# Performance work log

Hardware: AMD Instinct MI355X
Metric: run time of the kernel (lower is better)

Reference implementation:

```python
import jax, jax.numpy as jnp
import numpy as np

B, N = 1, 768
C_A, C_S, C_Z = 768, 384, 128
H, C_HID, N_TRANS = 16, 48, 2
INF = 1e9
PNAMES = ['attn_s_ln_g', 'attn_ada_gate_w', 'attn_ada_gate_b', 'attn_ada_skip_w',
          'wq', 'bq', 'wk', 'wv', 'z_ln_g', 'z_ln_b', 'wb', 'wg', 'wo',
          'attn_out_gate_w', 'attn_out_gate_b',
          'tr_s_ln_g', 'tr_ada_gate_w', 'tr_ada_gate_b', 'tr_ada_skip_w',
          'tr_w1', 'tr_w2', 'tr_wo', 'tr_out_gate_w', 'tr_out_gate_b']


def _ln(x, eps=1e-5):
    mu = jnp.mean(x, axis=-1, keepdims=True)
    var = jnp.mean((x - mu) ** 2, axis=-1, keepdims=True)
    return (x - mu) * jax.lax.rsqrt(var + eps)


def _adaln(a, s, s_g, gate_w, gate_b, skip_w):
    # AF3 Algorithm 26 AdaLN: a <- LN(a, no affine); s <- LN(s, scale only)
    a_ln = _ln(a)
    s_ln = _ln(s) * s_g
    return jax.nn.sigmoid(s_ln @ gate_w + gate_b) * a_ln + s_ln @ skip_w


def setup_inputs() -> dict:
    key = jax.random.key(0)
    ks = iter(jax.random.split(key, 40))
    w = lambda *sh: jax.random.normal(next(ks), sh, jnp.float32) * 0.02
    return dict(
        a=jax.random.normal(next(ks), (B, N, C_A), jnp.float32),
        s=jax.random.normal(next(ks), (B, N, C_S), jnp.float32),
        z=jax.random.normal(next(ks), (B, N, N, C_Z), jnp.float32),
        mask=jnp.ones((B, N), jnp.int32),
        attn_s_ln_g=jnp.ones((C_S,), jnp.float32),
        attn_ada_gate_w=w(C_S, C_A),
        attn_ada_gate_b=jnp.zeros((C_A,), jnp.float32),
        attn_ada_skip_w=w(C_S, C_A),
        wq=w(C_A, H * C_HID), bq=jnp.zeros((H * C_HID,), jnp.float32),
        wk=w(C_A, H * C_HID), wv=w(C_A, H * C_HID),
        z_ln_g=jnp.ones((C_Z,), jnp.float32), z_ln_b=jnp.zeros((C_Z,), jnp.float32),
        wb=w(C_Z, H), wg=w(C_A, H * C_HID), wo=w(H * C_HID, C_A),
        attn_out_gate_w=w(C_S, C_A),
        attn_out_gate_b=jnp.full((C_A,), -2.0, jnp.float32),  # AdaLN-Zero bias init -2
        tr_s_ln_g=jnp.ones((C_S,), jnp.float32),
        tr_ada_gate_w=w(C_S, C_A),
        tr_ada_gate_b=jnp.zeros((C_A,), jnp.float32),
        tr_ada_skip_w=w(C_S, C_A),
        tr_w1=w(C_A, N_TRANS * C_A), tr_w2=w(C_A, N_TRANS * C_A),
        tr_wo=w(N_TRANS * C_A, C_A),
        tr_out_gate_w=w(C_S, C_A),
        tr_out_gate_b=jnp.full((C_A,), -2.0, jnp.float32),
    )


def _block(a, s, z, maskf, p):
    # --- AttentionPairBias (AF3 Alg 24), residual ---
    a_ln = _adaln(a, s, p['attn_s_ln_g'], p['attn_ada_gate_w'],
                  p['attn_ada_gate_b'], p['attn_ada_skip_w'])
    q = (a_ln @ p['wq'] + p['bq']).reshape(B, N, H, C_HID)
    k = (a_ln @ p['wk']).reshape(B, N, H, C_HID)
    v = (a_ln @ p['wv']).reshape(B, N, H, C_HID)
    pair_bias = (_ln(z) * p['z_ln_g'] + p['z_ln_b']) @ p['wb']  # [B,N,N,H]
    logits = jnp.einsum('bqhc,bkhc->bhqk', q, k) / np.float32(np.sqrt(C_HID))
    logits = logits + jnp.moveaxis(pair_bias, -1, 1)
    logits = logits + (maskf - 1.0)[:, None, None, :] * INF  # mask over keys
    attn = jax.nn.softmax(logits, axis=-1)
    o = jnp.einsum('bhqk,bkhc->bqhc', attn, v)
    g = jax.nn.sigmoid(a_ln @ p['wg']).reshape(B, N, H, C_HID)
    o = (o * g).reshape(B, N, H * C_HID) @ p['wo']
    o = jax.nn.sigmoid(s @ p['attn_out_gate_w'] + p['attn_out_gate_b']) * o
    a = a + o
    # --- ConditionedTransitionBlock (AF3 Alg 25, SwiGLU), residual ---
    t_ln = _adaln(a, s, p['tr_s_ln_g'], p['tr_ada_gate_w'],
                  p['tr_ada_gate_b'], p['tr_ada_skip_w'])
    hid = jax.nn.silu(t_ln @ p['tr_w1']) * (t_ln @ p['tr_w2'])
    t = jax.nn.sigmoid(s @ p['tr_out_gate_w'] + p['tr_out_gate_b']) * (hid @ p['tr_wo'])
    t = t * maskf[..., None]  # _mask_trans=True
    return a + t


def reference(a, s, z, mask, attn_s_ln_g, attn_ada_gate_w, attn_ada_gate_b,
              attn_ada_skip_w, wq, bq, wk, wv, z_ln_g, z_ln_b, wb, wg, wo,
              attn_out_gate_w, attn_out_gate_b, tr_s_ln_g, tr_ada_gate_w,
              tr_ada_gate_b, tr_ada_skip_w, tr_w1, tr_w2, tr_wo,
              tr_out_gate_w, tr_out_gate_b):
    p = dict(zip(PNAMES, (attn_s_ln_g, attn_ada_gate_w, attn_ada_gate_b,
                          attn_ada_skip_w, wq, bq, wk, wv, z_ln_g, z_ln_b, wb,
                          wg, wo, attn_out_gate_w, attn_out_gate_b, tr_s_ln_g,
                          tr_ada_gate_w, tr_ada_gate_b, tr_ada_skip_w, tr_w1,
                          tr_w2, tr_wo, tr_out_gate_w, tr_out_gate_b)))
    return _block(a, s, z, mask.astype(a.dtype), p)
```

## Files before the change

### kernel.cpp

```cpp
#include <hip/hip_runtime.h>
#include <hip/hip_bf16.h>
#include <stdint.h>


typedef __bf16 bf16x8 __attribute__((ext_vector_type(8)));
typedef float  f32x4  __attribute__((ext_vector_type(4)));

#define DEVI __device__ __forceinline__

DEVI uint16_t f2b(float f){ __hip_bfloat16 h = __float2bfloat16(f); return __builtin_bit_cast(uint16_t, h); }
DEVI float    b2f(uint16_t u){ return __bfloat162float(__builtin_bit_cast(__hip_bfloat16, u)); }
DEVI float    sigm(float x){ return 1.0f/(1.0f + __expf(-x)); }

DEVI f32x4 MFMA(uint4 a, uint4 b, f32x4 c){
  return __builtin_amdgcn_mfma_f32_16x16x32_bf16(
      __builtin_bit_cast(bf16x8, a), __builtin_bit_cast(bf16x8, b), c, 0, 0, 0);
}

constexpr size_t SZ_BT_ADA   = (size_t)1536*384*2;
constexpr size_t OFF_BT_ADA_ATTN = 0;
constexpr size_t OFF_BT_ADA_TR   = OFF_BT_ADA_ATTN + SZ_BT_ADA;
constexpr size_t OFF_BT_OUTGATE  = OFF_BT_ADA_TR   + SZ_BT_ADA;
constexpr size_t OFF_BT_QKVG     = OFF_BT_OUTGATE  + SZ_BT_ADA;
constexpr size_t OFF_BT_WO       = OFF_BT_QKVG + (size_t)3072*768*2;
constexpr size_t OFF_BT_W12      = OFF_BT_WO   + (size_t)768*768*2;
constexpr size_t OFF_BT_TRWO     = OFF_BT_W12  + (size_t)3072*768*2;
constexpr size_t OFF_WBGT        = OFF_BT_TRWO + (size_t)768*1536*2;
constexpr size_t OFF_ZCOL        = OFF_WBGT + 4096;
constexpr size_t OFF_OGB         = OFF_ZCOL + 256;
constexpr size_t OFF_SBF         = OFF_OGB + 6144;
constexpr size_t OFF_SLNA        = OFF_SBF  + (size_t)768*384*2;
constexpr size_t OFF_SLNT        = OFF_SLNA + (size_t)768*384*2;
constexpr size_t OFF_ALNRAW      = OFF_SLNT + (size_t)768*384*2;
constexpr size_t OFF_GATEOUT     = OFF_ALNRAW + (size_t)768*768*4;
constexpr size_t OFF_GS          = OFF_GATEOUT + (size_t)768*1536*4;
constexpr size_t OFF_ALNBF       = OFF_GS + (size_t)768*1536*4;
constexpr size_t OFF_QKVG        = OFF_ALNBF + (size_t)768*768*2;
constexpr size_t OFF_QP          = OFF_QKVG + (size_t)768*3072*4;
constexpr size_t OFF_KP          = OFF_QP + (size_t)16*768*64*2;
constexpr size_t OFF_VT          = OFF_KP + (size_t)16*768*64*2;
constexpr size_t OFF_BIAS        = OFF_VT + (size_t)16*64*768*2;
constexpr size_t OFF_SP          = OFF_BIAS + (size_t)16*768*768*2;
constexpr size_t OFF_OBF         = OFF_SP + (size_t)16*768*768*2;
constexpr size_t OFF_AMID        = OFF_OBF + (size_t)768*768*2;

struct CvtArgs {
  const float* src[14];
  uint16_t*    dst[14];
  int K[14], N[14];
  int prefix[15];
};

__global__ __launch_bounds__(256) void k_cvt(CvtArgs a){
  int bid = blockIdx.x;
  int ti = 0;
  while (ti < 13 && bid >= a.prefix[ti+1]) ti++;
  int local = bid - a.prefix[ti];
  int K = a.K[ti], N = a.N[ti];
  int tN = N >> 5;
  int n0 = (local % tN) << 5, k0 = (local / tN) << 5;
  __shared__ float lds[32][33];
  const float* src = a.src[ti];
  uint16_t* dst = a.dst[ti];
  int t = threadIdx.x;
  int c = t & 31, r0 = t >> 5;
  #pragma unroll
  for (int i = 0; i < 4; i++){
    int kk = r0 + 8*i;
    lds[kk][c] = src[(size_t)(k0+kk)*N + n0 + c];
  }
  __syncthreads();
  #pragma unroll
  for (int i = 0; i < 4; i++){
    int nn = r0 + 8*i;
    dst[(size_t)(n0+nn)*K + k0 + c] = f2b(lds[c][nn]);
  }
}

__global__ __launch_bounds__(128) void k_prep(
    const float* s, const float* g_attn, const float* g_tr,
    const float* attn_ogb, const float* tr_ogb,
    const float* z_g, const float* z_b, const float* wb,
    uint16_t* s_bf, uint16_t* sln_a, uint16_t* sln_t,
    float* ogb, uint16_t* wbgt, float* zcol)
{
  int b = blockIdx.x, t = threadIdx.x;
  if (b < 768){
    const float* row = s + (size_t)b*384;
    float x0 = row[t], x1 = row[t+128], x2 = row[t+256];
    float sm = x0+x1+x2, sq = x0*x0+x1*x1+x2*x2;
    #pragma unroll
    for (int off = 32; off; off >>= 1){ sm += __shfl_xor(sm, off, 64); sq += __shfl_xor(sq, off, 64); }
    __shared__ float rs_[2], rq_[2];
    int w = t >> 6;
    if ((t & 63) == 0){ rs_[w] = sm; rq_[w] = sq; }
    __syncthreads();
    float S = rs_[0]+rs_[1], Q = rq_[0]+rq_[1];
    float mu = S * (1.f/384.f);
    float var = Q * (1.f/384.f) - mu*mu;
    float rstd = rsqrtf(var + 1e-5f);
    float xs[3] = {x0, x1, x2};
    #pragma unroll
    for (int i = 0; i < 3; i++){
      int ci = t + 128*i;
      float ln = (xs[i] - mu) * rstd;
      s_bf [(size_t)b*384 + ci] = f2b(xs[i]);
      sln_a[(size_t)b*384 + ci] = f2b(ln * g_attn[ci]);
      sln_t[(size_t)b*384 + ci] = f2b(ln * g_tr[ci]);
    }
  } else if (b == 768){
    for (int i = t; i < 1536; i += 128)
      ogb[i] = (i < 768) ? attn_ogb[i] : tr_ogb[i-768];
  } else {
    for (int i = t; i < 2048; i += 128){
      int h = i >> 7, c = i & 127;
      wbgt[i] = f2b(z_g[c] * wb[c*16 + h]);
    }
    if (t < 16){
      float cs = 0.f, cn = 0.f;
      for (int c = 0; c < 128; c++){ cs += z_g[c]*wb[c*16+t]; cn += z_b[c]*wb[c*16+t]; }
      zcol[t] = cs; zcol[16+t] = cn;
    }
  }
}

__global__ __launch_bounds__(256) void k_ln768(const float* in, float* out){
  int b = blockIdx.x, t = threadIdx.x;
  const float* row = in + (size_t)b*768;
  float x0 = row[t], x1 = row[t+256], x2 = row[t+512];
  float sm = x0+x1+x2, sq = x0*x0+x1*x1+x2*x2;
  #pragma unroll
  for (int off = 32; off; off >>= 1){ sm += __shfl_xor(sm, off, 64); sq += __shfl_xor(sq, off, 64); }
  __shared__ float rs_[4], rq_[4];
  int w = t >> 6;
  if ((t & 63) == 0){ rs_[w] = sm; rq_[w] = sq; }
  __syncthreads();
  float S = rs_[0]+rs_[1]+rs_[2]+rs_[3], Q = rq_[0]+rq_[1]+rq_[2]+rq_[3];
  float mu = S*(1.f/768.f), var = Q*(1.f/768.f) - mu*mu, rstd = rsqrtf(var + 1e-5f);
  float* orow = out + (size_t)b*768;
  orow[t]     = (x0-mu)*rstd;
  orow[t+256] = (x1-mu)*rstd;
  orow[t+512] = (x2-mu)*rstd;
}

__global__ __launch_bounds__(256) void k_gemm(
    const uint16_t* __restrict__ A, const uint16_t* __restrict__ BT,
    int M, int N, int K,
    float* outF, uint16_t* outB, int mode,
    const float* bias, const float* gate, int gateLd, int gateOff,
    const float* resid, const int* mask)
{
  constexpr int SA = 40;
  __shared__ uint16_t As[64*SA], Bs[64*SA];
  int t = threadIdx.x;
  int n0 = blockIdx.x*64, m0 = blockIdx.y*64;
  int w = t >> 6, lane = t & 63, mm = lane & 15, q = lane >> 4;
  f32x4 zz = {0.f, 0.f, 0.f, 0.f};
  f32x4 acc[4] = {zz, zz, zz, zz};
  int r = t >> 2, c4 = t & 3;
  const uint4* Ag = (const uint4*)(A + (size_t)(m0 + r)*K) + c4;
  const uint4* Bg = (const uint4*)(BT + (size_t)(n0 + r)*K) + c4;
  for (int k0 = 0; k0 < K; k0 += 32){
    *(uint4*)&As[r*SA + c4*8] = Ag[k0 >> 3];
    *(uint4*)&Bs[r*SA + c4*8] = Bg[k0 >> 3];
    __syncthreads();
    uint4 av = *(const uint4*)&As[(16*w + mm)*SA + q*8];
    #pragma unroll
    for (int j = 0; j < 4; j++){
      uint4 bv = *(const uint4*)&Bs[(16*j + mm)*SA + q*8];
      acc[j] = MFMA(av, bv, acc[j]);
    }
    __syncthreads();
  }
  #pragma unroll
  for (int j = 0; j < 4; j++){
    #pragma unroll
    for (int rr = 0; rr < 4; rr++){
      int row = m0 + 16*w + q*4 + rr;
      int col = n0 + 16*j + mm;
      float v = acc[j][rr];
      size_t oi = (size_t)row*N + col;
      if (mode == 0)      outF[oi] = v;
      else if (mode == 1) outB[oi] = f2b(v);
      else if (mode == 2) outF[oi] = sigm(v + bias[col]);
      else if (mode == 5) outF[oi] = resid[oi] + gate[(size_t)row*gateLd + gateOff + col]*v;
      else {
        float mf = (float)mask[row];
        outF[oi] = resid[oi] + mf * gate[(size_t)row*gateLd + gateOff + col] * v;
      }
    }
  }
}

__global__ __launch_bounds__(256) void k_zbias(
    const float* __restrict__ z, const uint16_t* __restrict__ wbgt_g,
    const float* __restrict__ zcol, uint16_t* __restrict__ bias_g)
{
  __shared__ uint16_t zb[64*128];
  __shared__ uint16_t wbt[16*128];
  __shared__ float mu_s[64], rs_s[64];
  __shared__ uint16_t Sout[16*72];
  int t = threadIdx.x;
  size_t P0 = (size_t)blockIdx.y*768 + (size_t)blockIdx.x*64;
  ((uint4*)wbt)[t] = ((const uint4*)wbgt_g)[t];
  int p = t >> 2, qq = t & 3;
  const float4* zp = (const float4*)(z + (P0 + p)*128) + qq*8;
  float s1 = 0.f, s2 = 0.f;
  uint32_t lb[16];
  #pragma unroll
  for (int it = 0; it < 8; it++){
    float4 v = zp[it];
    s1 += v.x + v.y + v.z + v.w;
    s2 += v.x*v.x + v.y*v.y + v.z*v.z + v.w*v.w;
    lb[2*it]   = (uint32_t)f2b(v.x) | ((uint32_t)f2b(v.y) << 16);
    lb[2*it+1] = (uint32_t)f2b(v.z) | ((uint32_t)f2b(v.w) << 16);
  }
  uint4* zb4 = (uint4*)zb;
  #pragma unroll
  for (int kk = 0; kk < 4; kk++)
    zb4[p*16 + qq*4 + kk] = ((uint4*)lb)[kk];
  s1 += __shfl_xor(s1, 1, 64); s1 += __shfl_xor(s1, 2, 64);
  s2 += __shfl_xor(s2, 1, 64); s2 += __shfl_xor(s2, 2, 64);
  if (qq == 0){
    float mu = s1 * (1.f/128.f);
    mu_s[p] = mu;
    rs_s[p] = rsqrtf(s2*(1.f/128.f) - mu*mu + 1e-5f);
  }
  __syncthreads();
  int w = t >> 6, lane = t & 63, hh = lane & 15, q = lane >> 4;
  float cs = zcol[hh], cn = zcol[16 + hh];
  f32x4 acc = {0.f, 0.f, 0.f, 0.f};
  const uint4* wbt4 = (const uint4*)wbt;
  #pragma unroll
  for (int kc = 0; kc < 4; kc++){
    uint4 av = zb4[(16*w + hh)*16 + kc*4 + q];
    uint4 bv = wbt4[hh*16 + kc*4 + q];
    acc = MFMA(av, bv, acc);
  }
  #pragma unroll
  for (int rr = 0; rr < 4; rr++){
    int pl = 16*w + q*4 + rr;
    float val = rs_s[pl]*(acc[rr] - mu_s[pl]*cs) + cn;
    Sout[hh*72 + pl] = f2b(val);
  }
  __syncthreads();
  int h2 = t >> 4, p2 = (t & 15)*4;
  uint2 v2 = *(uint2*)&Sout[h2*72 + p2];
  *(uint2*)(bias_g + (size_t)h2*589824 + P0 + p2) = v2;
}

__global__ __launch_bounds__(256) void k_trans(
    const float* __restrict__ qkvg, const float* __restrict__ bq,
    uint16_t* qp, uint16_t* kp, uint16_t* vt)
{
  int h = blockIdx.y, n0 = blockIdx.x*64, t = threadIdx.x;
  __shared__ uint16_t vbuf[64*72];
  int c = t & 63, r0 = t >> 6;
  const float scale = 0.14433756729740643f;
  for (int r = r0; r < 64; r += 4){
    size_t base = (size_t)(n0 + r)*3072;
    float qv = 0.f, kv = 0.f, vv = 0.f;
    if (c < 48){
      int cc = h*48 + c;
      qv = (qkvg[base + cc] + bq[cc]) * scale;
      kv = qkvg[base + 768 + cc];
      vv = qkvg[base + 1536 + cc];
    }
    size_t oi = ((size_t)h*768 + n0 + r)*64 + c;
    qp[oi] = f2b(qv);
    kp[oi] = f2b(kv);
    vbuf[c*72 + r] = f2b(vv);
  }
  __syncthreads();
  int cc = t >> 2, rb = (t & 3)*16;
  uint16_t* dst = vt + ((size_t)h*64 + cc)*768 + n0 + rb;
  *(uint4*)dst       = *(uint4*)&vbuf[cc*72 + rb];
  *(uint4*)(dst + 8) = *(uint4*)&vbuf[cc*72 + rb + 8];
}

__global__ __launch_bounds__(256) void k_logits(
    const uint16_t* __restrict__ qp, const uint16_t* __restrict__ kp,
    const uint16_t* __restrict__ bias_g, const int* __restrict__ mask,
    uint16_t* __restrict__ SP)
{
  int h = blockIdx.z, q0 = blockIdx.y*64, k0 = blockIdx.x*64;
  constexpr int SA = 72;
  __shared__ uint16_t Qs[64*SA], Ks[64*SA];
  int t = threadIdx.x;
  int r = t >> 2, c4 = t & 3;
  const uint4* Qg = (const uint4*)(qp + ((size_t)h*768 + q0 + r)*64);
  const uint4* Kg = (const uint4*)(kp + ((size_t)h*768 + k0 + r)*64);
  *(uint4*)&Qs[r*SA + c4*8]       = Qg[c4];
  *(uint4*)&Qs[r*SA + (c4+4)*8]   = Qg[c4+4];
  *(uint4*)&Ks[r*SA + c4*8]       = Kg[c4];
  *(uint4*)&Ks[r*SA + (c4+4)*8]   = Kg[c4+4];
  __syncthreads();
  int w = t >> 6, lane = t & 63, mm = lane & 15, q = lane >> 4;
  f32x4 zz = {0.f,0.f,0.f,0.f};
  f32x4 acc[4] = {zz, zz, zz, zz};
  #pragma unroll
  for (int kc = 0; kc < 2; kc++){
    uint4 av = *(const uint4*)&Qs[(16*w + mm)*SA + kc*32 + q*8];
    #pragma unroll
    for (int j = 0; j < 4; j++){
      uint4 bv = *(const uint4*)&Ks[(16*j + mm)*SA + kc*32 + q*8];
      acc[j] = MFMA(av, bv, acc[j]);
    }
  }
  #pragma unroll
  for (int j = 0; j < 4; j++){
    #pragma unroll
    for (int rr = 0; rr < 4; rr++){
      int row = q0 + 16*w + q*4 + rr;
      int col = k0 + 16*j + mm;
      size_t bi = (size_t)h*589824 + (size_t)row*768 + col;
      float v = acc[j][rr] + b2f(bias_g[bi]) + ((float)mask[col] - 1.f)*1e9f;
      SP[bi] = f2b(v);
    }
  }
}

__global__ __launch_bounds__(256) void k_softmax(uint16_t* SP){
  size_t base = (size_t)blockIdx.x * 768;
  int t = threadIdx.x;
  float x0 = b2f(SP[base+t]), x1 = b2f(SP[base+t+256]), x2 = b2f(SP[base+t+512]);
  float mx = fmaxf(x0, fmaxf(x1, x2));
  #pragma unroll
  for (int off = 32; off; off >>= 1) mx = fmaxf(mx, __shfl_xor(mx, off, 64));
  __shared__ float rm[4], rsum[4];
  int w = t >> 6;
  if ((t & 63) == 0) rm[w] = mx;
  __syncthreads();
  mx = fmaxf(fmaxf(rm[0], rm[1]), fmaxf(rm[2], rm[3]));
  float e0 = __expf(x0 - mx), e1 = __expf(x1 - mx), e2 = __expf(x2 - mx);
  float sm = e0 + e1 + e2;
  #pragma unroll
  for (int off = 32; off; off >>= 1) sm += __shfl_xor(sm, off, 64);
  if ((t & 63) == 0) rsum[w] = sm;
  __syncthreads();
  sm = rsum[0]+rsum[1]+rsum[2]+rsum[3];
  float inv = 1.f / sm;
  SP[base+t]     = f2b(e0*inv);
  SP[base+t+256] = f2b(e1*inv);
  SP[base+t+512] = f2b(e2*inv);
}

__global__ __launch_bounds__(256) void k_pv(
    const uint16_t* __restrict__ SP, const uint16_t* __restrict__ vt,
    const float* __restrict__ qkvg, uint16_t* __restrict__ obf)
{
  int h = blockIdx.y, q0 = blockIdx.x*64;
  constexpr int SA = 40;
  __shared__ uint16_t Ps[64*SA], Vs[64*SA];
  int t = threadIdx.x;
  int r = t >> 2, c4 = t & 3;
  int w = t >> 6, lane = t & 63, mm = lane & 15, q = lane >> 4;
  const uint16_t* Pbase = SP + (size_t)h*589824;
  const uint16_t* Vbase = vt + (size_t)h*64*768;
  f32x4 zz = {0.f,0.f,0.f,0.f};
  f32x4 acc[3] = {zz, zz, zz};
  for (int k0 = 0; k0 < 768; k0 += 32){
    *(uint4*)&Ps[r*SA + c4*8] = *((const uint4*)(Pbase + (size_t)(q0 + r)*768 + k0) + c4);
    *(uint4*)&Vs[r*SA + c4*8] = *((const uint4*)(Vbase + (size_t)r*768 + k0) + c4);
    __syncthreads();
    uint4 av = *(const uint4*)&Ps[(16*w + mm)*SA + q*8];
    #pragma unroll
    for (int j = 0; j < 3; j++){
      uint4 bv = *(const uint4*)&Vs[(16*j + mm)*SA + q*8];
      acc[j] = MFMA(av, bv, acc[j]);
    }
    __syncthreads();
  }
  #pragma unroll
  for (int j = 0; j < 3; j++){
    #pragma unroll
    for (int rr = 0; rr < 4; rr++){
      int col = 16*j + mm;
      if (col < 48){
        int row = q0 + 16*w + q*4 + rr;
        float g = qkvg[(size_t)row*3072 + 2304 + h*48 + col];
        obf[(size_t)row*768 + h*48 + col] = f2b(acc[j][rr] * sigm(g));
      }
    }
  }
}

__global__ __launch_bounds__(256) void k_adaln(
    const float* __restrict__ gs, const float* __restrict__ gb,
    const float* __restrict__ alnraw, uint16_t* __restrict__ aln)
{
  int idx4 = blockIdx.x*256 + threadIdx.x;
  int row = idx4 / 192;
  int c4 = (idx4 % 192)*4;
  float4 g4 = *(const float4*)(gs + (size_t)row*1536 + c4);
  float4 s4 = *(const float4*)(gs + (size_t)row*1536 + 768 + c4);
  float4 a4 = *(const float4*)(alnraw + (size_t)row*768 + c4);
  float4 b4 = *(const float4*)(gb + c4);
  uint32_t lo = (uint32_t)f2b(sigm(g4.x + b4.x)*a4.x + s4.x)
              | ((uint32_t)f2b(sigm(g4.y + b4.y)*a4.y + s4.y) << 16);
  uint32_t hi = (uint32_t)f2b(sigm(g4.z + b4.z)*a4.z + s4.z)
              | ((uint32_t)f2b(sigm(g4.w + b4.w)*a4.w + s4.w) << 16);
  uint2 uv; uv.x = lo; uv.y = hi;
  *(uint2*)(aln + (size_t)row*768 + c4) = uv;
}

__global__ __launch_bounds__(256) void k_silu(const float* __restrict__ h12, uint16_t* __restrict__ hid){
  int idx4 = blockIdx.x*256 + threadIdx.x;
  int row = idx4 / 384;
  int c4 = (idx4 % 384)*4;
  float4 x1 = *(const float4*)(h12 + (size_t)row*3072 + c4);
  float4 x2 = *(const float4*)(h12 + (size_t)row*3072 + 1536 + c4);
  uint32_t lo = (uint32_t)f2b(x1.x*sigm(x1.x)*x2.x)
              | ((uint32_t)f2b(x1.y*sigm(x1.y)*x2.y) << 16);
  uint32_t hi = (uint32_t)f2b(x1.z*sigm(x1.z)*x2.z)
              | ((uint32_t)f2b(x1.w*sigm(x1.w)*x2.w) << 16);
  uint2 uv; uv.x = lo; uv.y = hi;
  *(uint2*)(hid + (size_t)row*1536 + c4) = uv;
}

extern "C" void kernel_launch(void* const* d_in, const int* in_sizes, int n_in,
                              void* d_out, int out_size, void* d_ws, size_t ws_size,
                              hipStream_t stream)
{
  const float* a            = (const float*)d_in[0];
  const float* s            = (const float*)d_in[1];
  const float* z            = (const float*)d_in[2];
  const int*   mask         = (const int*)  d_in[3];
  const float* attn_s_ln_g  = (const float*)d_in[4];
  const float* attn_gate_w  = (const float*)d_in[5];
  const float* attn_gate_b  = (const float*)d_in[6];
  const float* attn_skip_w  = (const float*)d_in[7];
  const float* wq           = (const float*)d_in[8];
  const float* bq           = (const float*)d_in[9];
  const float* wk           = (const float*)d_in[10];
  const float* wv           = (const float*)d_in[11];
  const float* z_ln_g       = (const float*)d_in[12];
  const float* z_ln_b       = (const float*)d_in[13];
  const float* wb           = (const float*)d_in[14];
  const float* wg           = (const float*)d_in[15];
  const float* wo           = (const float*)d_in[16];
  const float* attn_og_w    = (const float*)d_in[17];
  const float* attn_og_b    = (const float*)d_in[18];
  const float* tr_s_ln_g    = (const float*)d_in[19];
  const float* tr_gate_w    = (const float*)d_in[20];
  const float* tr_gate_b    = (const float*)d_in[21];
  const float* tr_skip_w    = (const float*)d_in[22];
  const float* tr_w1        = (const float*)d_in[23];
  const float* tr_w2        = (const float*)d_in[24];
  const float* tr_wo        = (const float*)d_in[25];
  const float* tr_og_w      = (const float*)d_in[26];
  const float* tr_og_b      = (const float*)d_in[27];

  char* wsb = (char*)d_ws;
  uint16_t* BTa   = (uint16_t*)(wsb + OFF_BT_ADA_ATTN);
  uint16_t* BTt   = (uint16_t*)(wsb + OFF_BT_ADA_TR);
  uint16_t* BTo   = (uint16_t*)(wsb + OFF_BT_OUTGATE);
  uint16_t* BTq   = (uint16_t*)(wsb + OFF_BT_QKVG);
  uint16_t* BTwo  = (uint16_t*)(wsb + OFF_BT_WO);
  uint16_t* BTw12 = (uint16_t*)(wsb + OFF_BT_W12);
  uint16_t* BTtw  = (uint16_t*)(wsb + OFF_BT_TRWO);
  uint16_t* WBGT  = (uint16_t*)(wsb + OFF_WBGT);
  float*    ZCOL  = (float*)   (wsb + OFF_ZCOL);
  float*    OGB   = (float*)   (wsb + OFF_OGB);
  uint16_t* SBF   = (uint16_t*)(wsb + OFF_SBF);
  uint16_t* SLNA  = (uint16_t*)(wsb + OFF_SLNA);
  uint16_t* SLNT  = (uint16_t*)(wsb + OFF_SLNT);
  float*    ALNRAW= (float*)   (wsb + OFF_ALNRAW);
  float*    GATEOUT=(float*)   (wsb + OFF_GATEOUT);
  float*    GS    = (float*)   (wsb + OFF_GS);
  uint16_t* ALNBF = (uint16_t*)(wsb + OFF_ALNBF);
  float*    QKVG  = (float*)   (wsb + OFF_QKVG);
  uint16_t* QP    = (uint16_t*)(wsb + OFF_QP);
  uint16_t* KP    = (uint16_t*)(wsb + OFF_KP);
  uint16_t* VT    = (uint16_t*)(wsb + OFF_VT);
  uint16_t* BIASB = (uint16_t*)(wsb + OFF_BIAS);
  uint16_t* SPB   = (uint16_t*)(wsb + OFF_SP);
  uint16_t* OBF   = (uint16_t*)(wsb + OFF_OBF);
  float*    AMID  = (float*)   (wsb + OFF_AMID);
  uint16_t* HIDBF = (uint16_t*)(wsb + OFF_BIAS);
  float*    OUTF  = (float*)d_out;

  CvtArgs ca;
  const float* srcs[14] = {attn_gate_w, attn_skip_w, tr_gate_w, tr_skip_w,
                           attn_og_w, tr_og_w, wq, wk, wv, wg, wo, tr_w1, tr_w2, tr_wo};
  uint16_t* dsts[14] = {BTa, BTa + (size_t)768*384, BTt, BTt + (size_t)768*384,
                        BTo, BTo + (size_t)768*384,
                        BTq, BTq + (size_t)768*768, BTq + (size_t)2*768*768, BTq + (size_t)3*768*768,
                        BTwo, BTw12, BTw12 + (size_t)1536*768, BTtw};
  int Ks[14] = {384,384,384,384,384,384, 768,768,768,768,768, 768,768, 1536};
  int Ns[14] = {768,768,768,768,768,768, 768,768,768,768,768, 1536,1536, 768};
  int tiles[14] = {288,288,288,288,288,288, 576,576,576,576,576, 1152,1152, 1152};
  int pre = 0;
  for (int i = 0; i < 14; i++){
    ca.src[i] = srcs[i]; ca.dst[i] = dsts[i]; ca.K[i] = Ks[i]; ca.N[i] = Ns[i];
    ca.prefix[i] = pre; pre += tiles[i];
  }
  ca.prefix[14] = pre;

  k_cvt<<<pre, 256, 0, stream>>>(ca);
  k_prep<<<770, 128, 0, stream>>>(s, attn_s_ln_g, tr_s_ln_g, attn_og_b, tr_og_b,
                                  z_ln_g, z_ln_b, wb, SBF, SLNA, SLNT, OGB, WBGT, ZCOL);
  k_ln768<<<768, 256, 0, stream>>>(a, ALNRAW);

  k_gemm<<<dim3(24,12), 256, 0, stream>>>(SBF, BTo, 768, 1536, 384,
      GATEOUT, nullptr, 2, OGB, nullptr, 0, 0, nullptr, nullptr);
  k_gemm<<<dim3(24,12), 256, 0, stream>>>(SLNA, BTa, 768, 1536, 384,
      GS, nullptr, 0, nullptr, nullptr, 0, 0, nullptr, nullptr);
  k_adaln<<<576, 256, 0, stream>>>(GS, attn_gate_b, ALNRAW, ALNBF);
  k_gemm<<<dim3(48,12), 256, 0, stream>>>(ALNBF, BTq, 768, 3072, 768,
      QKVG, nullptr, 0, nullptr, nullptr, 0, 0, nullptr, nullptr);

  k_zbias<<<dim3(12,768), 256, 0, stream>>>(z, WBGT, ZCOL, BIASB);
  k_trans<<<dim3(12,16), 256, 0, stream>>>(QKVG, bq, QP, KP, VT);
  k_logits<<<dim3(12,12,16), 256, 0, stream>>>(QP, KP, BIASB, mask, SPB);
  k_softmax<<<12288, 256, 0, stream>>>(SPB);
  k_pv<<<dim3(12,16), 256, 0, stream>>>(SPB, VT, QKVG, OBF);
  k_gemm<<<dim3(12,12), 256, 0, stream>>>(OBF, BTwo, 768, 768, 768,
      AMID, nullptr, 5, nullptr, GATEOUT, 1536, 0, a, nullptr);

  k_ln768<<<768, 256, 0, stream>>>(AMID, ALNRAW);
  k_gemm<<<dim3(24,12), 256, 0, stream>>>(SLNT, BTt, 768, 1536, 384,
      GS, nullptr, 0, nullptr, nullptr, 0, 0, nullptr, nullptr);
  k_adaln<<<576, 256, 0, stream>>>(GS, tr_gate_b, ALNRAW, ALNBF);
  k_gemm<<<dim3(48,12), 256, 0, stream>>>(ALNBF, BTw12, 768, 3072, 768,
      QKVG, nullptr, 0, nullptr, nullptr, 0, 0, nullptr, nullptr);
  k_silu<<<1152, 256, 0, stream>>>(QKVG, HIDBF);
  k_gemm<<<dim3(12,12), 256, 0, stream>>>(HIDBF, BTtw, 768, 768, 1536,
      OUTF, nullptr, 4, nullptr, GATEOUT, 1536, 768, AMID, mask);
}
```

Before: 682.6 us.

## Fuse attention into flash kernel, fuse LN into AdaLN, bf16 intermediates, async GEMM loads

Result: faster. 635.3 us (-6.9%).

```diff
diff --git a/kernel.cpp b/kernel.cpp
--- a/kernel.cpp
+++ b/kernel.cpp
@@ -15,6 +15,12 @@
 DEVI f32x4 MFMA(uint4 a, uint4 b, f32x4 c){
   return __builtin_amdgcn_mfma_f32_16x16x32_bf16(
       __builtin_bit_cast(bf16x8, a), __builtin_bit_cast(bf16x8, b), c, 0, 0, 0);
+}
+
+DEVI void glds16(const void* g, void* l){
+  __builtin_amdgcn_global_load_lds(
+      (const __attribute__((address_space(1))) void*)g,
+      (__attribute__((address_space(3))) void*)l, 16, 0, 0);
 }
 
 constexpr size_t SZ_BT_ADA   = (size_t)1536*384*2;
@@ -31,17 +37,15 @@
 constexpr size_t OFF_SBF         = OFF_OGB + 6144;
 constexpr size_t OFF_SLNA        = OFF_SBF  + (size_t)768*384*2;
 constexpr size_t OFF_SLNT        = OFF_SLNA + (size_t)768*384*2;
-constexpr size_t OFF_ALNRAW      = OFF_SLNT + (size_t)768*384*2;
-constexpr size_t OFF_GATEOUT     = OFF_ALNRAW + (size_t)768*768*4;
+constexpr size_t OFF_GATEOUT     = OFF_SLNT + (size_t)768*384*2;
 constexpr size_t OFF_GS          = OFF_GATEOUT + (size_t)768*1536*4;
 constexpr size_t OFF_ALNBF       = OFF_GS + (size_t)768*1536*4;
-constexpr size_t OFF_QKVG        = OFF_ALNBF + (size_t)768*768*2;
-constexpr size_t OFF_QP          = OFF_QKVG + (size_t)768*3072*4;
+constexpr size_t OFF_QKVGB       = OFF_ALNBF + (size_t)768*768*2;
+constexpr size_t OFF_QP          = OFF_QKVGB + (size_t)768*3072*2;
 constexpr size_t OFF_KP          = OFF_QP + (size_t)16*768*64*2;
 constexpr size_t OFF_VT          = OFF_KP + (size_t)16*768*64*2;
 constexpr size_t OFF_BIAS        = OFF_VT + (size_t)16*64*768*2;
-constexpr size_t OFF_SP          = OFF_BIAS + (size_t)16*768*768*2;
-constexpr size_t OFF_OBF         = OFF_SP + (size_t)16*768*768*2;
+constexpr size_t OFF_OBF         = OFF_BIAS + (size_t)16*768*768*2;
 constexpr size_t OFF_AMID        = OFF_OBF + (size_t)768*768*2;
 
 struct CvtArgs {
@@ -124,9 +128,12 @@
   }
 }
 
-__global__ __launch_bounds__(256) void k_ln768(const float* in, float* out){
+__global__ __launch_bounds__(256) void k_adaln2(
+    const float* __restrict__ asrc, const float* __restrict__ gs,
+    const float* __restrict__ gb, uint16_t* __restrict__ out)
+{
   int b = blockIdx.x, t = threadIdx.x;
-  const float* row = in + (size_t)b*768;
+  const float* row = asrc + (size_t)b*768;
   float x0 = row[t], x1 = row[t+256], x2 = row[t+512];
   float sm = x0+x1+x2, sq = x0*x0+x1*x1+x2*x2;
   #pragma unroll
@@ -137,10 +144,14 @@
   __syncthreads();
   float S = rs_[0]+rs_[1]+rs_[2]+rs_[3], Q = rq_[0]+rq_[1]+rq_[2]+rq_[3];
   float mu = S*(1.f/768.f), var = Q*(1.f/768.f) - mu*mu, rstd = rsqrtf(var + 1e-5f);
-  float* orow = out + (size_t)b*768;
-  orow[t]     = (x0-mu)*rstd;
-  orow[t+256] = (x1-mu)*rstd;
-  orow[t+512] = (x2-mu)*rstd;
+  float xs[3] = {x0, x1, x2};
+  #pragma unroll
+  for (int i = 0; i < 3; i++){
+    int c = t + 256*i;
+    float g  = gs[(size_t)b*1536 + c];
+    float sk = gs[(size_t)b*1536 + 768 + c];
+    out[(size_t)b*768 + c] = f2b(sigm(g + gb[c]) * ((xs[i]-mu)*rstd) + sk);
+  }
 }
 
 __global__ __launch_bounds__(256) void k_gemm(
@@ -150,27 +161,40 @@
     const float* bias, const float* gate, int gateLd, int gateOff,
     const float* resid, const int* mask)
 {
-  constexpr int SA = 40;
-  __shared__ uint16_t As[64*SA], Bs[64*SA];
+  __shared__ uint16_t As[64*64], Bs[64*64];
   int t = threadIdx.x;
   int n0 = blockIdx.x*64, m0 = blockIdx.y*64;
   int w = t >> 6, lane = t & 63, mm = lane & 15, q = lane >> 4;
-  f32x4 zz = {0.f, 0.f, 0.f, 0.f};
+  int fc0 = 128*w + lane, fc1 = fc0 + 64;
+  int r0 = fc0 >> 3, c0 = (fc0 & 7) ^ (r0 & 7);
+  int r1 = fc1 >> 3, c1 = (fc1 & 7) ^ (r1 & 7);
+  const uint16_t* gA0 = A  + (size_t)(m0 + r0)*K + c0*8;
+  const uint16_t* gA1 = A  + (size_t)(m0 + r1)*K + c1*8;
+  const uint16_t* gB0 = BT + (size_t)(n0 + r0)*K + c0*8;
+  const uint16_t* gB1 = BT + (size_t)(n0 + r1)*K + c1*8;
+  uint16_t* lA0 = As + (2*w + 0)*512;
+  uint16_t* lA1 = As + (2*w + 1)*512;
+  uint16_t* lB0 = Bs + (2*w + 0)*512;
+  uint16_t* lB1 = Bs + (2*w + 1)*512;
+  f32x4 zz = {0.f,0.f,0.f,0.f};
   f32x4 acc[4] = {zz, zz, zz, zz};
-  int r = t >> 2, c4 = t & 3;
-  const uint4* Ag = (const uint4*)(A + (size_t)(m0 + r)*K) + c4;
-  const uint4* Bg = (const uint4*)(BT + (size_t)(n0 + r)*K) + c4;
-  for (int k0 = 0; k0 < K; k0 += 32){
-    *(uint4*)&As[r*SA + c4*8] = Ag[k0 >> 3];
-    *(uint4*)&Bs[r*SA + c4*8] = Bg[k0 >> 3];
+  int sw = mm & 7;
+  for (int k0 = 0; k0 < K; k0 += 64){
     __syncthreads();
-    uint4 av = *(const uint4*)&As[(16*w + mm)*SA + q*8];
-    #pragma unroll
-    for (int j = 0; j < 4; j++){
-      uint4 bv = *(const uint4*)&Bs[(16*j + mm)*SA + q*8];
-      acc[j] = MFMA(av, bv, acc[j]);
-    }
+    glds16(gA0 + k0, lA0);
+    glds16(gA1 + k0, lA1);
+    glds16(gB0 + k0, lB0);
+    glds16(gB1 + k0, lB1);
     __syncthreads();
+    #pragma unroll
+    for (int kc = 0; kc < 2; kc++){
+      uint4 av = *(const uint4*)&As[(16*w + mm)*64 + ((kc*4 + q) ^ sw)*8];
+      #pragma unroll
+      for (int j = 0; j < 4; j++){
+        uint4 bv = *(const uint4*)&Bs[(16*j + mm)*64 + ((kc*4 + q) ^ sw)*8];
+        acc[j] = MFMA(av, bv, acc[j]);
+      }
+    }
   }
   #pragma unroll
   for (int j = 0; j < 4; j++){
@@ -250,7 +274,7 @@
 }
 
 __global__ __launch_bounds__(256) void k_trans(
-    const float* __restrict__ qkvg, const float* __restrict__ bq,
+    const uint16_t* __restrict__ qkvg, const float* __restrict__ bq,
     uint16_t* qp, uint16_t* kp, uint16_t* vt)
 {
   int h = blockIdx.y, n0 = blockIdx.x*64, t = threadIdx.x;
@@ -262,9 +286,9 @@
     float qv = 0.f, kv = 0.f, vv = 0.f;
     if (c < 48){
       int cc = h*48 + c;
-      qv = (qkvg[base + cc] + bq[cc]) * scale;
-      kv = qkvg[base + 768 + cc];
-      vv = qkvg[base + 1536 + cc];
+      qv = (b2f(qkvg[base + cc]) + bq[cc]) * scale;
+      kv = b2f(qkvg[base + 768 + cc]);
+      vv = b2f(qkvg[base + 1536 + cc]);
     }
     size_t oi = ((size_t)h*768 + n0 + r)*64 + c;
     qp[oi] = f2b(qv);
@@ -278,144 +302,138 @@
   *(uint4*)(dst + 8) = *(uint4*)&vbuf[cc*72 + rb + 8];
 }
 
-__global__ __launch_bounds__(256) void k_logits(
+__global__ __launch_bounds__(256) void k_flash(
     const uint16_t* __restrict__ qp, const uint16_t* __restrict__ kp,
-    const uint16_t* __restrict__ bias_g, const int* __restrict__ mask,
-    uint16_t* __restrict__ SP)
-{
-  int h = blockIdx.z, q0 = blockIdx.y*64, k0 = blockIdx.x*64;
-  constexpr int SA = 72;
-  __shared__ uint16_t Qs[64*SA], Ks[64*SA];
+    const uint16_t* __restrict__ vt, const uint16_t* __restrict__ bias_g,
+    const uint16_t* __restrict__ qkvg, const int* __restrict__ mask,
+    uint16_t* __restrict__ obf)
+{
+  __shared__ uint16_t Qs[64*72], Ks[64*72], Vs[64*72], Ps[64*72];
+  __shared__ float mk[768];
   int t = threadIdx.x;
-  int r = t >> 2, c4 = t & 3;
-  const uint4* Qg = (const uint4*)(qp + ((size_t)h*768 + q0 + r)*64);
-  const uint4* Kg = (const uint4*)(kp + ((size_t)h*768 + k0 + r)*64);
-  *(uint4*)&Qs[r*SA + c4*8]       = Qg[c4];
-  *(uint4*)&Qs[r*SA + (c4+4)*8]   = Qg[c4+4];
-  *(uint4*)&Ks[r*SA + c4*8]       = Kg[c4];
-  *(uint4*)&Ks[r*SA + (c4+4)*8]   = Kg[c4+4];
-  __syncthreads();
+  int q0 = blockIdx.x*64, h = blockIdx.y;
   int w = t >> 6, lane = t & 63, mm = lane & 15, q = lane >> 4;
+  {
+    int row = t >> 2, c = t & 3;
+    const uint4* src = (const uint4*)(qp + ((size_t)h*768 + q0 + row)*64) + c*2;
+    *(uint4*)&Qs[row*72 + c*16]     = src[0];
+    *(uint4*)&Qs[row*72 + c*16 + 8] = src[1];
+    mk[t] = (float)mask[t]; mk[t+256] = (float)mask[t+256]; mk[t+512] = (float)mask[t+512];
+  }
   f32x4 zz = {0.f,0.f,0.f,0.f};
-  f32x4 acc[4] = {zz, zz, zz, zz};
-  #pragma unroll
-  for (int kc = 0; kc < 2; kc++){
-    uint4 av = *(const uint4*)&Qs[(16*w + mm)*SA + kc*32 + q*8];
+  f32x4 o0 = zz, o1 = zz, o2 = zz;
+  f32x4 m_i = {-1e30f,-1e30f,-1e30f,-1e30f};
+  f32x4 l_i = zz;
+  const uint16_t* bias_h = bias_g + (size_t)h*589824;
+  for (int kt = 0; kt < 12; kt++){
+    __syncthreads();
+    {
+      int row = t >> 2, c = t & 3;
+      const uint4* ks = (const uint4*)(kp + ((size_t)h*768 + kt*64 + row)*64) + c*2;
+      *(uint4*)&Ks[row*72 + c*16]     = ks[0];
+      *(uint4*)&Ks[row*72 + c*16 + 8] = ks[1];
+      const uint4* vs = (const uint4*)(vt + ((size_t)h*64 + row)*768 + kt*64) + c*2;
+      *(uint4*)&Vs[row*72 + c*16]     = vs[0];
+      *(uint4*)&Vs[row*72 + c*16 + 8] = vs[1];
+    }
+    __syncthreads();
+    f32x4 s[4] = {zz, zz, zz, zz};
+    #pragma unroll
+    for (int kc = 0; kc < 2; kc++){
+      uint4 av = *(const uint4*)&Qs[(16*w + mm)*72 + kc*32 + q*8];
+      #pragma unroll
+      for (int j = 0; j < 4; j++){
+        uint4 bv = *(const uint4*)&Ks[(16*j + mm)*72 + kc*32 + q*8];
+        s[j] = MFMA(av, bv, s[j]);
+      }
+    }
+    int srow = q0 + 16*w + q*4;
     #pragma unroll
     for (int j = 0; j < 4; j++){
-      uint4 bv = *(const uint4*)&Ks[(16*j + mm)*SA + kc*32 + q*8];
-      acc[j] = MFMA(av, bv, acc[j]);
-    }
-  }
-  #pragma unroll
-  for (int j = 0; j < 4; j++){
+      int scol = kt*64 + 16*j + mm;
+      float mt = (mk[scol] - 1.f)*1e9f;
+      #pragma unroll
+      for (int rr = 0; rr < 4; rr++)
+        s[j][rr] += b2f(bias_h[(size_t)(srow+rr)*768 + scol]) + mt;
+    }
+    f32x4 tm = s[0];
+    #pragma unroll
+    for (int j = 1; j < 4; j++)
+      #pragma unroll
+      for (int rr = 0; rr < 4; rr++) tm[rr] = fmaxf(tm[rr], s[j][rr]);
+    #pragma unroll
+    for (int off = 1; off < 16; off <<= 1)
+      #pragma unroll
+      for (int rr = 0; rr < 4; rr++) tm[rr] = fmaxf(tm[rr], __shfl_xor(tm[rr], off, 64));
+    f32x4 mnew, alpha, rsum = zz;
+    #pragma unroll
+    for (int rr = 0; rr < 4; rr++){
+      mnew[rr] = fmaxf(m_i[rr], tm[rr]);
+      alpha[rr] = __expf(m_i[rr] - mnew[rr]);
+    }
+    #pragma unroll
+    for (int j = 0; j < 4; j++)
+      #pragma unroll
+      for (int rr = 0; rr < 4; rr++){
+        s[j][rr] = __expf(s[j][rr] - mnew[rr]);
+        rsum[rr] += s[j][rr];
+      }
+    #pragma unroll
+    for (int off = 1; off < 16; off <<= 1)
+      #pragma unroll
+      for (int rr = 0; rr < 4; rr++) rsum[rr] += __shfl_xor(rsum[rr], off, 64);
+    #pragma unroll
+    for (int rr = 0; rr < 4; rr++){
+      l_i[rr] = l_i[rr]*alpha[rr] + rsum[rr];
+      o0[rr] *= alpha[rr]; o1[rr] *= alpha[rr]; o2[rr] *= alpha[rr];
+      m_i[rr] = mnew[rr];
+    }
+    #pragma unroll
+    for (int j = 0; j < 4; j++)
+      #pragma unroll
+      for (int rr = 0; rr < 4; rr++)
+        Ps[(16*w + q*4 + rr)*72 + 16*j + mm] = f2b(s[j][rr]);
+    __syncthreads();
+    #pragma unroll
+    for (int kc = 0; kc < 2; kc++){
+      uint4 av = *(const uint4*)&Ps[(16*w + mm)*72 + kc*32 + q*8];
+      uint4 bv0 = *(const uint4*)&Vs[(mm)*72      + kc*32 + q*8];
+      uint4 bv1 = *(const uint4*)&Vs[(16+mm)*72   + kc*32 + q*8];
+      uint4 bv2 = *(const uint4*)&Vs[(32+mm)*72   + kc*32 + q*8];
+      o0 = MFMA(av, bv0, o0);
+      o1 = MFMA(av, bv1, o1);
+      o2 = MFMA(av, bv2, o2);
+    }
+  }
+  f32x4 inv;
+  #pragma unroll
+  for (int rr = 0; rr < 4; rr++) inv[rr] = 1.f / l_i[rr];
+  #pragma unroll
+  for (int j = 0; j < 3; j++){
+    f32x4 ov = (j == 0) ? o0 : (j == 1) ? o1 : o2;
+    int col = 16*j + mm;
     #pragma unroll
     for (int rr = 0; rr < 4; rr++){
       int row = q0 + 16*w + q*4 + rr;
-      int col = k0 + 16*j + mm;
-      size_t bi = (size_t)h*589824 + (size_t)row*768 + col;
-      float v = acc[j][rr] + b2f(bias_g[bi]) + ((float)mask[col] - 1.f)*1e9f;
-      SP[bi] = f2b(v);
-    }
-  }
-}
-
-__global__ __launch_bounds__(256) void k_softmax(uint16_t* SP){
-  size_t base = (size_t)blockIdx.x * 768;
-  int t = threadIdx.x;
-  float x0 = b2f(SP[base+t]), x1 = b2f(SP[base+t+256]), x2 = b2f(SP[base+t+512]);
-  float mx = fmaxf(x0, fmaxf(x1, x2));
-  #pragma unroll
-  for (int off = 32; off; off >>= 1) mx = fmaxf(mx, __shfl_xor(mx, off, 64));
-  __shared__ float rm[4], rsum[4];
-  int w = t >> 6;
-  if ((t & 63) == 0) rm[w] = mx;
-  __syncthreads();
-  mx = fmaxf(fmaxf(rm[0], rm[1]), fmaxf(rm[2], rm[3]));
-  float e0 = __expf(x0 - mx), e1 = __expf(x1 - mx), e2 = __expf(x2 - mx);
-  float sm = e0 + e1 + e2;
-  #pragma unroll
-  for (int off = 32; off; off >>= 1) sm += __shfl_xor(sm, off, 64);
-  if ((t & 63) == 0) rsum[w] = sm;
-  __syncthreads();
-  sm = rsum[0]+rsum[1]+rsum[2]+rsum[3];
-  float inv = 1.f / sm;
-  SP[base+t]     = f2b(e0*inv);
-  SP[base+t+256] = f2b(e1*inv);
-  SP[base+t+512] = f2b(e2*inv);
-}
-
-__global__ __launch_bounds__(256) void k_pv(
-    const uint16_t* __restrict__ SP, const uint16_t* __restrict__ vt,
-    const float* __restrict__ qkvg, uint16_t* __restrict__ obf)
-{
-  int h = blockIdx.y, q0 = blockIdx.x*64;
-  constexpr int SA = 40;
-  __shared__ uint16_t Ps[64*SA], Vs[64*SA];
-  int t = threadIdx.x;
-  int r = t >> 2, c4 = t & 3;
-  int w = t >> 6, lane = t & 63, mm = lane & 15, q = lane >> 4;
-  const uint16_t* Pbase = SP + (size_t)h*589824;
-  const uint16_t* Vbase = vt + (size_t)h*64*768;
-  f32x4 zz = {0.f,0.f,0.f,0.f};
-  f32x4 acc[3] = {zz, zz, zz};
-  for (int k0 = 0; k0 < 768; k0 += 32){
-    *(uint4*)&Ps[r*SA + c4*8] = *((const uint4*)(Pbase + (size_t)(q0 + r)*768 + k0) + c4);
-    *(uint4*)&Vs[r*SA + c4*8] = *((const uint4*)(Vbase + (size_t)r*768 + k0) + c4);
-    __syncthreads();
-    uint4 av = *(const uint4*)&Ps[(16*w + mm)*SA + q*8];
-    #pragma unroll
-    for (int j = 0; j < 3; j++){
-      uint4 bv = *(const uint4*)&Vs[(16*j + mm)*SA + q*8];
-      acc[j] = MFMA(av, bv, acc[j]);
-    }
-    __syncthreads();
-  }
-  #pragma unroll
-  for (int j = 0; j < 3; j++){
-    #pragma unroll
-    for (int rr = 0; rr < 4; rr++){
-      int col = 16*j + mm;
-      if (col < 48){
-        int row = q0 + 16*w + q*4 + rr;
-        float g = qkvg[(size_t)row*3072 + 2304 + h*48 + col];
-        obf[(size_t)row*768 + h*48 + col] = f2b(acc[j][rr] * sigm(g));
-      }
-    }
-  }
-}
-
-__global__ __launch_bounds__(256) void k_adaln(
-    const float* __restrict__ gs, const float* __restrict__ gb,
-    const float* __restrict__ alnraw, uint16_t* __restrict__ aln)
-{
-  int idx4 = blockIdx.x*256 + threadIdx.x;
-  int row = idx4 / 192;
-  int c4 = (idx4 % 192)*4;
-  float4 g4 = *(const float4*)(gs + (size_t)row*1536 + c4);
-  float4 s4 = *(const float4*)(gs + (size_t)row*1536 + 768 + c4);
-  float4 a4 = *(const float4*)(alnraw + (size_t)row*768 + c4);
-  float4 b4 = *(const float4*)(gb + c4);
-  uint32_t lo = (uint32_t)f2b(sigm(g4.x + b4.x)*a4.x + s4.x)
-              | ((uint32_t)f2b(sigm(g4.y + b4.y)*a4.y + s4.y) << 16);
-  uint32_t hi = (uint32_t)f2b(sigm(g4.z + b4.z)*a4.z + s4.z)
-              | ((uint32_t)f2b(sigm(g4.w + b4.w)*a4.w + s4.w) << 16);
-  uint2 uv; uv.x = lo; uv.y = hi;
-  *(uint2*)(aln + (size_t)row*768 + c4) = uv;
-}
-
-__global__ __launch_bounds__(256) void k_silu(const float* __restrict__ h12, uint16_t* __restrict__ hid){
+      float g = b2f(qkvg[(size_t)row*3072 + 2304 + h*48 + col]);
+      obf[(size_t)row*768 + h*48 + col] = f2b(ov[rr]*inv[rr]*sigm(g));
+    }
+  }
+}
+
+__global__ __launch_bounds__(256) void k_silu(const uint16_t* __restrict__ h12, uint16_t* __restrict__ hid){
   int idx4 = blockIdx.x*256 + threadIdx.x;
   int row = idx4 / 384;
   int c4 = (idx4 % 384)*4;
-  float4 x1 = *(const float4*)(h12 + (size_t)row*3072 + c4);
-  float4 x2 = *(const float4*)(h12 + (size_t)row*3072 + 1536 + c4);
-  uint32_t lo = (uint32_t)f2b(x1.x*sigm(x1.x)*x2.x)
-              | ((uint32_t)f2b(x1.y*sigm(x1.y)*x2.y) << 16);
-  uint32_t hi = (uint32_t)f2b(x1.z*sigm(x1.z)*x2.z)
-              | ((uint32_t)f2b(x1.w*sigm(x1.w)*x2.w) << 16);
-  uint2 uv; uv.x = lo; uv.y = hi;
-  *(uint2*)(hid + (size_t)row*1536 + c4) = uv;
+  const uint16_t* p1 = h12 + (size_t)row*3072 + c4;
+  const uint16_t* p2 = p1 + 1536;
+  uint16_t o[4];
+  #pragma unroll
+  for (int i = 0; i < 4; i++){
+    float x1 = b2f(p1[i]), x2 = b2f(p2[i]);
+    o[i] = f2b(x1*sigm(x1)*x2);
+  }
+  *(uint2*)(hid + (size_t)row*1536 + c4) = *(uint2*)o;
 }
 
 extern "C" void kernel_launch(void* const* d_in, const int* in_sizes, int n_in,
@@ -465,16 +483,14 @@
   uint16_t* SBF   = (uint16_t*)(wsb + OFF_SBF);
   uint16_t* SLNA  = (uint16_t*)(wsb + OFF_SLNA);
   uint16_t* SLNT  = (uint16_t*)(wsb + OFF_SLNT);
-  float*    ALNRAW= (float*)   (wsb + OFF_ALNRAW);
   float*    GATEOUT=(float*)   (wsb + OFF_GATEOUT);
   float*    GS    = (float*)   (wsb + OFF_GS);
   uint16_t* ALNBF = (uint16_t*)(wsb + OFF_ALNBF);
-  float*    QKVG  = (float*)   (wsb + OFF_QKVG);
+  uint16_t* QKVGB = (uint16_t*)(wsb + OFF_QKVGB);
   uint16_t* QP    = (uint16_t*)(wsb + OFF_QP);
   uint16_t* KP    = (uint16_t*)(wsb + OFF_KP);
   uint16_t* VT    = (uint16_t*)(wsb + OFF_VT);
   uint16_t* BIASB = (uint16_t*)(wsb + OFF_BIAS);
-  uint16_t* SPB   = (uint16_t*)(wsb + OFF_SP);
   uint16_t* OBF   = (uint16_t*)(wsb + OFF_OBF);
   float*    AMID  = (float*)   (wsb + OFF_AMID);
   uint16_t* HIDBF = (uint16_t*)(wsb + OFF_BIAS);
@@ -500,31 +516,27 @@
   k_cvt<<<pre, 256, 0, stream>>>(ca);
   k_prep<<<770, 128, 0, stream>>>(s, attn_s_ln_g, tr_s_ln_g, attn_og_b, tr_og_b,
                                   z_ln_g, z_ln_b, wb, SBF, SLNA, SLNT, OGB, WBGT, ZCOL);
-  k_ln768<<<768, 256, 0, stream>>>(a, ALNRAW);
 
   k_gemm<<<dim3(24,12), 256, 0, stream>>>(SBF, BTo, 768, 1536, 384,
       GATEOUT, nullptr, 2, OGB, nullptr, 0, 0, nullptr, nullptr);
   k_gemm<<<dim3(24,12), 256, 0, stream>>>(SLNA, BTa, 768, 1536, 384,
       GS, nullptr, 0, nullptr, nullptr, 0, 0, nullptr, nullptr);
-  k_adaln<<<576, 256, 0, stream>>>(GS, attn_gate_b, ALNRAW, ALNBF);
+  k_adaln2<<<768, 256, 0, stream>>>(a, GS, attn_gate_b, ALNBF);
   k_gemm<<<dim3(48,12), 256, 0, stream>>>(ALNBF, BTq, 768, 3072, 768,
-      QKVG, nullptr, 0, nullptr, nullptr, 0, 0, nullptr, nullptr);
+      nullptr, QKVGB, 1, nullptr, nullptr, 0, 0, nullptr, nullptr);
 
   k_zbias<<<dim3(12,768), 256, 0, stream>>>(z, WBGT, ZCOL, BIASB);
-  k_trans<<<dim3(12,16), 256, 0, stream>>>(QKVG, bq, QP, KP, VT);
-  k_logits<<<dim3(12,12,16), 256, 0, stream>>>(QP, KP, BIASB, mask, SPB);
-  k_softmax<<<12288, 256, 0, stream>>>(SPB);
-  k_pv<<<dim3(12,16), 256, 0, stream>>>(SPB, VT, QKVG, OBF);
+  k_trans<<<dim3(12,16), 256, 0, stream>>>(QKVGB, bq, QP, KP, VT);
+  k_flash<<<dim3(12,16), 256, 0, stream>>>(QP, KP, VT, BIASB, QKVGB, mask, OBF);
   k_gemm<<<dim3(12,12), 256, 0, stream>>>(OBF, BTwo, 768, 768, 768,
       AMID, nullptr, 5, nullptr, GATEOUT, 1536, 0, a, nullptr);
 
-  k_ln768<<<768, 256, 0, stream>>>(AMID, ALNRAW);
   k_gemm<<<dim3(24,12), 256, 0, stream>>>(SLNT, BTt, 768, 1536, 384,
       GS, nullptr, 0, nullptr, nullptr, 0, 0, nullptr, nullptr);
-  k_adaln<<<576, 256, 0, stream>>>(GS, tr_gate_b, ALNRAW, ALNBF);
+  k_adaln2<<<768, 256, 0, stream>>>(AMID, GS, tr_gate_b, ALNBF);
   k_gemm<<<dim3(48,12), 256, 0, stream>>>(ALNBF, BTw12, 768, 3072, 768,
-      QKVG, nullptr, 0, nullptr, nullptr, 0, 0, nullptr, nullptr);
-  k_silu<<<1152, 256, 0, stream>>>(QKVG, HIDBF);
+      nullptr, QKVGB, 1, nullptr, nullptr, 0, 0, nullptr, nullptr);
+  k_silu<<<1152, 256, 0, stream>>>(QKVGB, HIDBF);
   k_gemm<<<dim3(12,12), 256, 0, stream>>>(HIDBF, BTtw, 768, 768, 1536,
       OUTF, nullptr, 4, nullptr, GATEOUT, 1536, 768, AMID, mask);
 }
```
